# Kernel tuning notes

Hardware: AMD Instinct MI355X
Metric: run time of the kernel (lower is better)

The kernel has to match this reference:

```python
import math
import jax, jax.numpy as jnp
import numpy as np

B, T, C, H = 4, 2048, 1024, 16

def _rope_cos_sin(dim, max_pos):
    half = dim // 2
    pos = jnp.arange(max_pos, dtype=jnp.float32)[:, None]
    freqs = jnp.exp(jnp.arange(half, dtype=jnp.float32) * (-math.log(10000.0) / (half - 1)))[None, :]
    args = pos * freqs  # [T, half]
    return jnp.cos(args), jnp.sin(args)

def _apply_rope(x, cos, sin):
    # x: [B, H, T, D]; pairs (even, odd) along D form complex numbers
    xr = x[..., 0::2]
    xi = x[..., 1::2]
    c = cos[None, None, :, :]
    s = sin[None, None, :, :]
    out_r = xr * c - xi * s
    out_i = xr * s + xi * c
    return jnp.stack([out_r, out_i], axis=-1).reshape(x.shape)

def setup_inputs() -> dict:
    key = jax.random.key(0)
    ks = jax.random.split(key, 9)
    sc = 1.0 / math.sqrt(C)
    return {
        "x": jax.random.normal(ks[0], (B, T, C), jnp.float32),
        "Wq": jax.random.normal(ks[1], (C, C), jnp.float32) * sc,
        "bq": jax.random.normal(ks[2], (C,), jnp.float32) * 0.01,
        "Wk": jax.random.normal(ks[3], (C, C), jnp.float32) * sc,
        "bk": jax.random.normal(ks[4], (C,), jnp.float32) * 0.01,
        "Wv": jax.random.normal(ks[5], (C, C), jnp.float32) * sc,
        "bv": jax.random.normal(ks[6], (C,), jnp.float32) * 0.01,
        "Wp": jax.random.normal(ks[7], (C, C), jnp.float32) * sc,
        "bp": jax.random.normal(ks[8], (C,), jnp.float32) * 0.01,
        "n_head": H,
    }

def reference(x, Wq, bq, Wk, bk, Wv, bv, Wp, bp, n_head):
    Bx, Tx, Cx = x.shape
    D = Cx // n_head
    def heads(w, b):
        return (x @ w + b).reshape(Bx, Tx, n_head, D).transpose(0, 2, 1, 3)  # [B,H,T,D]
    q = heads(Wq, bq)
    k = heads(Wk, bk)
    v = heads(Wv, bv)
    cos, sin = _rope_cos_sin(D, Tx)
    q = _apply_rope(q, cos, sin)
    k = _apply_rope(k, cos, sin)
    att = jnp.einsum("bhtd,bhsd->bhts", q, k) * (1.0 / math.sqrt(D))
    causal = jnp.tril(jnp.ones((Tx, Tx), dtype=bool))
    att = jnp.where(causal[None, None, :, :], att, jnp.float32(-1e10))
    att = jax.nn.softmax(att, axis=-1)
    y = jnp.einsum("bhts,bhsd->bhtd", att, v)
    y = y.transpose(0, 2, 1, 3).reshape(Bx, Tx, Cx)
    return y @ Wp + bp
```

## Files before the change

kernel.cpp:

```cpp
#include <hip/hip_runtime.h>
#include <hip/hip_bf16.h>
#include <stdint.h>

namespace {

constexpr int Bx = 4, Tx = 2048, Cx = 1024, Hx = 16, Dx = 64;
constexpr int Mx = Bx * Tx;

typedef __attribute__((ext_vector_type(8))) short bf16x8;
typedef __attribute__((ext_vector_type(4))) float f32x4;
typedef __attribute__((ext_vector_type(16))) float f32x16;
typedef __attribute__((ext_vector_type(2))) unsigned int u32x2;

__device__ __forceinline__ float b2f(unsigned short u) {
  unsigned int v = ((unsigned int)u) << 16;
  return __builtin_bit_cast(float, v);
}
__device__ __forceinline__ unsigned short f2b(float f) {
  unsigned int v = __builtin_bit_cast(unsigned int, f);
  v += 0x7fffu + ((v >> 16) & 1u);
  return (unsigned short)(v >> 16);
}
__device__ __forceinline__ uint32_t pkbf(float a, float b) {
  __hip_bfloat162 h = __float22bfloat162_rn(float2{a, b});
  uint32_t r;
  __builtin_memcpy(&r, &h, 4);
  return r;
}
__device__ __forceinline__ void pl32swap(uint32_t& a, uint32_t& b) {
  u32x2 r = __builtin_amdgcn_permlane32_swap(a, b, false, false);
  a = r[0];
  b = r[1];
}

#define GLD16(g, lp) __builtin_amdgcn_global_load_lds(                     \
    (__attribute__((address_space(1))) void*)(g),                          \
    (__attribute__((address_space(3))) void*)(lp), 16, 0, 0)

__global__ void ca_cvt(const float* __restrict__ src, unsigned short* __restrict__ dst, int n4) {
  int i = blockIdx.x * blockDim.x + threadIdx.x;
  int stride = gridDim.x * blockDim.x;
  for (; i < n4; i += stride) {
    float4 f = ((const float4*)src)[i];
    ushort4 o;
    o.x = f2b(f.x); o.y = f2b(f.y); o.z = f2b(f.z); o.w = f2b(f.w);
    ((ushort4*)dst)[i] = o;
  }
}

__global__ void ca_wt(const float* __restrict__ W, unsigned short* __restrict__ Wt) {
  __shared__ float tile[32][33];
  int n0 = blockIdx.x * 32, k0 = blockIdx.y * 32;
  int j = threadIdx.x & 31, i = threadIdx.x >> 5;
#pragma unroll
  for (int r = 0; r < 4; ++r)
    tile[i + 8 * r][j] = W[(size_t)(k0 + i + 8 * r) * Cx + n0 + j];
  __syncthreads();
#pragma unroll
  for (int r = 0; r < 4; ++r)
    Wt[(size_t)(n0 + i + 8 * r) * Cx + k0 + j] = f2b(tile[j][i + 8 * r]);
}

__global__ void ca_rtab(float* __restrict__ ct, float* __restrict__ st) {
  int idx = blockIdx.x * blockDim.x + threadIdx.x;
  int t = idx >> 5, i = idx & 31;
  float fr = expf((float)i * -0.29710775393471563f);
  float a = (float)t * fr;
  ct[idx] = cosf(a);
  st[idx] = sinf(a);
}

template <int MODE>
__global__ __launch_bounds__(256) void ca_gemm(
    const unsigned short* __restrict__ A, const unsigned short* __restrict__ Bt,
    const float* __restrict__ b0, const float* __restrict__ b1, const float* __restrict__ b2,
    const float* __restrict__ ctab, const float* __restrict__ stab,
    void* __restrict__ out, int M, int N, int K) {
  __shared__ __align__(16) unsigned short Al[2][128 * 32];
  __shared__ __align__(16) unsigned short Bl[2][128 * 32];
  int tid = threadIdx.x;
  int w = tid >> 6, l = tid & 63;
  int m0 = blockIdx.x * 128, n0 = blockIdx.y * 128;
  int wm = (w >> 1) * 64, wn = (w & 1) * 64;
  f32x4 acc[4][4] = {};

  int lr = l & 15, lk8 = (l >> 4) * 8;
  int srow = w * 32 + (l >> 2), scol = (l & 3) * 8;
  const unsigned short* ga0 = A + (size_t)(m0 + srow) * K + scol;
  const unsigned short* gb0 = Bt + (size_t)(n0 + srow) * K + scol;
  int nk = K / 32;
  auto stage = [&](int kt, int buf) {
    const unsigned short* ga = ga0 + kt * 32;
    const unsigned short* gb = gb0 + kt * 32;
    unsigned short* la = &Al[buf][w * 1024];
    unsigned short* lb = &Bl[buf][w * 1024];
    GLD16(ga, la);
    GLD16(ga + (size_t)16 * K, la + 512);
    GLD16(gb, lb);
    GLD16(gb + (size_t)16 * K, lb + 512);
  };
  stage(0, 0);
  __syncthreads();
  int cur = 0;
  for (int kt = 0; kt < nk; ++kt) {
    if (kt + 1 < nk) stage(kt + 1, cur ^ 1);
    bf16x8 af[4], bfr[4];
#pragma unroll
    for (int mi = 0; mi < 4; ++mi)
      af[mi] = *(const bf16x8*)&Al[cur][(wm + mi * 16 + lr) * 32 + lk8];
#pragma unroll
    for (int ni = 0; ni < 4; ++ni)
      bfr[ni] = *(const bf16x8*)&Bl[cur][(wn + ni * 16 + lr) * 32 + lk8];
#pragma unroll
    for (int mi = 0; mi < 4; ++mi)
#pragma unroll
      for (int ni = 0; ni < 4; ++ni)
        acc[mi][ni] = __builtin_amdgcn_mfma_f32_16x16x32_bf16(af[mi], bfr[ni], acc[mi][ni], 0, 0, 0);
    __syncthreads();
    cur ^= 1;
  }

  int lq4 = (l >> 4) * 4;
  if (MODE == 0) {
    constexpr float SC = 0.18033688011112042f;
    int which = n0 >> 10;
    int nb = n0 & 1023;
    const float* bias = which == 0 ? b0 : (which == 1 ? b1 : b2);
    unsigned short* o = (unsigned short*)out + (size_t)which * M * 1024;
    bool doRope = which < 2;
    float scl = which == 0 ? SC : 1.0f;
#pragma unroll
    for (int mi = 0; mi < 4; ++mi)
#pragma unroll
      for (int ni = 0; ni < 4; ++ni) {
        int ncol = nb + wn + ni * 16 + lr;
        float bv = bias[ncol];
        int j = (ncol & 63) >> 1;
        bool even = (ncol & 1) == 0;
#pragma unroll
        for (int rg = 0; rg < 4; ++rg) {
          int m = m0 + wm + mi * 16 + lq4 + rg;
          float val = acc[mi][ni][rg] + bv;
          if (doRope) {
            int t = m & (Tx - 1);
            float c = ctab[t * 32 + j], s = stab[t * 32 + j];
            float other = __shfl_xor(val, 1);
            float res = even ? (val * c - other * s) : (other * s + val * c);
            val = res * scl;
          }
          o[(size_t)m * 1024 + ncol] = f2b(val);
        }
      }
  } else {
    float* o = (float*)out;
#pragma unroll
    for (int mi = 0; mi < 4; ++mi)
#pragma unroll
      for (int ni = 0; ni < 4; ++ni) {
        int ncol = n0 + wn + ni * 16 + lr;
        float bv = b0[ncol];
#pragma unroll
        for (int rg = 0; rg < 4; ++rg) {
          int m = m0 + wm + mi * 16 + lq4 + rg;
          o[(size_t)m * N + ncol] = acc[mi][ni][rg] + bv;
        }
      }
  }
}

__global__ void ca_vfl(const unsigned short* __restrict__ v, unsigned short* __restrict__ vfl) {
  __shared__ __align__(16) unsigned short tl[64][80];
  int t0 = blockIdx.x * 64;
  int bh = blockIdx.y;
  int b = bh >> 4, h = bh & 15;
  int tid = threadIdx.x;
  const unsigned short* vb = v + (size_t)b * Tx * Cx + h * Dx;
#pragma unroll
  for (int it = 0; it < 2; ++it) {
    int tt = it * 32 + (tid >> 3), d0 = (tid & 7) * 8;
    uint4 x = *(const uint4*)&vb[(size_t)(t0 + tt) * Cx + d0];
    unsigned short* u = (unsigned short*)&x;
#pragma unroll
    for (int jj = 0; jj < 8; ++jj) tl[d0 + jj][tt] = u[jj];
  }
  __syncthreads();
  int l = tid & 63, lo = l & 31, hi = l >> 5;
  int g = tid >> 6, tloc = g >> 1, kc = g & 1;
  int tglob = (t0 >> 5) + tloc;
  unsigned short* vo = vfl + ((size_t)bh * 64 + tglob) * 2048;
#pragma unroll
  for (int dc = 0; dc < 2; ++dc) {
    int j = dc * 2 + kc;
    uint4 x = *(const uint4*)&tl[dc * 32 + lo][tloc * 32 + hi * 8 + kc * 16];
    *(uint4*)(vo + j * 512 + l * 8) = x;
  }
}

__global__ __launch_bounds__(64) void ca_kfl(
    const unsigned short* __restrict__ k, unsigned short* __restrict__ kfl) {
  int l = threadIdx.x & 63;
  int bh = blockIdx.x, t = blockIdx.y;
  int b = bh >> 4, h = bh & 15;
  int lo = l & 31, hi = l >> 5;
  const unsigned short* kr = k + (size_t)b * Tx * Cx + h * Dx + (size_t)(t * 32 + lo) * Cx + hi * 8;
  unsigned short* ko = kfl + ((size_t)bh * 64 + t) * 2048;
#pragma unroll
  for (int c = 0; c < 4; ++c) {
    uint4 x = *(const uint4*)(kr + c * 16);
    *(uint4*)(ko + c * 512 + l * 8) = x;
  }
}

__global__ __launch_bounds__(64) void ca_attn(
    const unsigned short* __restrict__ q, const unsigned short* __restrict__ kfl,
    const unsigned short* __restrict__ vfl, unsigned short* __restrict__ y) {
  __shared__ uint32_t els[32][33];
  int l = threadIdx.x & 63;
  int bh = blockIdx.x;
  int qt = (int)gridDim.y - 1 - (int)blockIdx.y;
  int b = bh >> 4, h16 = bh & 15;
  const unsigned short* qp = q + (size_t)b * Tx * Cx + h16 * Dx;
  const unsigned short* kb = kfl + (size_t)bh * 64 * 2048 + l * 8;
  const unsigned short* vb = vfl + (size_t)bh * 64 * 2048 + l * 8;
  int lo = l & 31, hi = l >> 5;
  constexpr float SHIFT = 20.0f;
  const uint32_t one2 = 0x3F803F80u;
  uint4 onesw{one2, one2, one2, one2};
  bf16x8 ONES = __builtin_bit_cast(bf16x8, onesw);

  int qbase = qt * 32;

  bf16x8 qf[4];
  {
    const unsigned short* qr = qp + (size_t)(qbase + lo) * Cx + hi * 8;
#pragma unroll
    for (int c = 0; c < 4; ++c) qf[c] = *(const bf16x8*)(qr + c * 16);
  }

  f32x16 acc0 = {}, acc1 = {}, sacc = {};
  int nt = qt + 1;

  uint4 rk[4], rv[4];
  auto loadK = [&](int t) {
#pragma unroll
    for (int c = 0; c < 4; ++c) rk[c] = *(const uint4*)(kb + t * 2048 + c * 512);
  };
  auto loadV = [&](int t) {
#pragma unroll
    for (int j = 0; j < 4; ++j) rv[j] = *(const uint4*)(vb + t * 2048 + j * 512);
  };
  loadK(0);
  loadV(0);

  for (int t = 0; t < nt; ++t) {
    bf16x8 kf[4], vf[4];
#pragma unroll
    for (int c = 0; c < 4; ++c) kf[c] = __builtin_bit_cast(bf16x8, rk[c]);
#pragma unroll
    for (int c = 0; c < 4; ++c) vf[c] = __builtin_bit_cast(bf16x8, rv[c]);
    if (t + 1 < nt) { loadK(t + 1); loadV(t + 1); }

    __builtin_amdgcn_s_setprio(1);
    f32x16 s = {};
    s = __builtin_amdgcn_mfma_f32_32x32x16_bf16(kf[0], qf[0], s, 0, 0, 0);
    s = __builtin_amdgcn_mfma_f32_32x32x16_bf16(kf[1], qf[1], s, 0, 0, 0);
    s = __builtin_amdgcn_mfma_f32_32x32x16_bf16(kf[2], qf[2], s, 0, 0, 0);
    s = __builtin_amdgcn_mfma_f32_32x32x16_bf16(kf[3], qf[3], s, 0, 0, 0);
    __builtin_amdgcn_s_setprio(0);

    float p[16];
    if (t == nt - 1) {
#pragma unroll
      for (int r = 0; r < 16; ++r) {
        int kvr = (r & 3) + 8 * (r >> 2) + 4 * hi;
        p[r] = (kvr > lo) ? 0.f : exp2f(s[r] - SHIFT);
      }
    } else {
#pragma unroll
      for (int r = 0; r < 16; ++r) p[r] = exp2f(s[r] - SHIFT);
    }

    uint32_t pk[8];
#pragma unroll
    for (int i = 0; i < 8; ++i) pk[i] = pkbf(p[2 * i], p[2 * i + 1]);
    pl32swap(pk[0], pk[2]);
    pl32swap(pk[1], pk[3]);
    pl32swap(pk[4], pk[6]);
    pl32swap(pk[5], pk[7]);
    uint4 xw{pk[0], pk[1], pk[2], pk[3]}, yw{pk[4], pk[5], pk[6], pk[7]};
    bf16x8 PB0 = __builtin_bit_cast(bf16x8, xw);
    bf16x8 PB1 = __builtin_bit_cast(bf16x8, yw);
    __builtin_amdgcn_s_setprio(1);
    acc0 = __builtin_amdgcn_mfma_f32_32x32x16_bf16(vf[0], PB0, acc0, 0, 0, 0);
    acc1 = __builtin_amdgcn_mfma_f32_32x32x16_bf16(vf[2], PB0, acc1, 0, 0, 0);
    sacc = __builtin_amdgcn_mfma_f32_32x32x16_bf16(ONES, PB0, sacc, 0, 0, 0);
    acc0 = __builtin_amdgcn_mfma_f32_32x32x16_bf16(vf[1], PB1, acc0, 0, 0, 0);
    acc1 = __builtin_amdgcn_mfma_f32_32x32x16_bf16(vf[3], PB1, acc1, 0, 0, 0);
    sacc = __builtin_amdgcn_mfma_f32_32x32x16_bf16(ONES, PB1, sacc, 0, 0, 0);
    __builtin_amdgcn_s_setprio(0);
  }

  float rl = __builtin_amdgcn_rcpf(sacc[0]);
#pragma unroll
  for (int dc = 0; dc < 2; ++dc) {
    f32x16 a = dc ? acc1 : acc0;
#pragma unroll
    for (int i = 0; i < 8; ++i) {
      uint32_t pkd = pkbf(a[2 * i] * rl, a[2 * i + 1] * rl);
      int d2 = (i & 1) + 4 * (i >> 1) + 2 * hi + dc * 16;
      els[lo][d2] = pkd;
    }
  }
  __syncthreads();
  unsigned short* yp = y + (size_t)b * Tx * Cx + h16 * Dx;
#pragma unroll
  for (int pp = 0; pp < 16; ++pp) {
    int qr = 2 * pp + hi;
    uint32_t val = els[qr][lo];
    *(uint32_t*)(yp + (size_t)(qbase + qr) * Cx + lo * 2) = val;
  }
}

}

extern "C" void kernel_launch(void* const* d_in, const int* in_sizes, int n_in,
                              void* d_out, int out_size, void* d_ws, size_t ws_size,
                              hipStream_t stream) {
  const float* x = (const float*)d_in[0];
  const float* Wq = (const float*)d_in[1];
  const float* bq = (const float*)d_in[2];
  const float* Wk = (const float*)d_in[3];
  const float* bk = (const float*)d_in[4];
  const float* Wv = (const float*)d_in[5];
  const float* bv = (const float*)d_in[6];
  const float* Wp = (const float*)d_in[7];
  const float* bp = (const float*)d_in[8];

  unsigned short* xb = (unsigned short*)d_ws;
  unsigned short* wt = xb + (size_t)Mx * Cx;
  float* ct = (float*)(wt + (size_t)4 * Cx * Cx);
  float* st = ct + Tx * 32;
  unsigned short* qb = (unsigned short*)(st + Tx * 32);
  unsigned short* kb = qb + (size_t)Mx * Cx;
  unsigned short* vb = kb + (size_t)Mx * Cx;
  unsigned short* vT = vb + (size_t)Mx * Cx;
  unsigned short* yb = vT + (size_t)Mx * Cx;
  unsigned short* kfl = yb + (size_t)Mx * Cx;
  unsigned short* vfl = kfl + (size_t)64 * 64 * 2048;

  ca_cvt<<<dim3(2048), dim3(256), 0, stream>>>(x, xb, Mx * Cx / 4);
  ca_wt<<<dim3(32, 32), dim3(256), 0, stream>>>(Wq, wt + (size_t)0 * Cx * Cx);
  ca_wt<<<dim3(32, 32), dim3(256), 0, stream>>>(Wk, wt + (size_t)1 * Cx * Cx);
  ca_wt<<<dim3(32, 32), dim3(256), 0, stream>>>(Wv, wt + (size_t)2 * Cx * Cx);
  ca_wt<<<dim3(32, 32), dim3(256), 0, stream>>>(Wp, wt + (size_t)3 * Cx * Cx);
  ca_rtab<<<dim3(Tx * 32 / 256), dim3(256), 0, stream>>>(ct, st);

  ca_gemm<0><<<dim3(64, 24), dim3(256), 0, stream>>>(xb, wt, bq, bk, bv, ct, st, qb, Mx, 3072, Cx);
  ca_vfl<<<dim3(Tx / 64, Bx * Hx), dim3(256), 0, stream>>>(vb, vfl);
  ca_kfl<<<dim3(64, 64), dim3(64), 0, stream>>>(kb, kfl);
  ca_attn<<<dim3(64, 64), dim3(64), 0, stream>>>(qb, kfl, vfl, yb);
  ca_gemm<1><<<dim3(64, 8), dim3(256), 0, stream>>>(yb, wt + (size_t)3 * Cx * Cx, bp,
                                                    nullptr, nullptr, nullptr, nullptr,
                                                    d_out, Mx, Cx, Cx);
}
```

Baseline: 217.5 us.

## Replace QKV projection GEMM with 256x256-tile 8-wave kernel using direct-to-LDS loads

```diff
diff --git a/kernel.cpp b/kernel.cpp
--- a/kernel.cpp
+++ b/kernel.cpp
@@ -70,12 +70,130 @@
   st[idx] = sinf(a);
 }
 
-template <int MODE>
-__global__ __launch_bounds__(256) void ca_gemm(
+__global__ __launch_bounds__(512, 1) void ca_gemm8(
     const unsigned short* __restrict__ A, const unsigned short* __restrict__ Bt,
     const float* __restrict__ b0, const float* __restrict__ b1, const float* __restrict__ b2,
     const float* __restrict__ ctab, const float* __restrict__ stab,
-    void* __restrict__ out, int M, int N, int K) {
+    unsigned short* __restrict__ out) {
+  extern __shared__ unsigned short lds8[];
+  unsigned short* ldsA = lds8;
+  unsigned short* ldsB = lds8 + 32768;
+
+  int tid = threadIdx.x;
+  int w = tid >> 6, l = tid & 63;
+  int wr = w >> 2, wc = w & 3;
+
+  int bid = (int)blockIdx.x;
+  int wgid = (bid & 7) * 48 + (bid >> 3);
+  int m0 = (wgid & 31) * 256;
+  int n0 = (wgid >> 5) * 256;
+
+  const unsigned short* aSrc = A + (size_t)(m0 + w * 8 + (l >> 3)) * Cx + (((l & 7) ^ (l >> 3)) * 8);
+  const unsigned short* bSrc = Bt + (size_t)(n0 + w * 8 + (l >> 3)) * Cx + (((l & 7) ^ (l >> 3)) * 8);
+  int dstRow = w * 8;
+
+  auto stageQ = [&](int ktn, int q, int buf) {
+    int half = q & 1;
+    size_t roff = (size_t)(half * 128) * Cx + ktn * 64;
+    if (q < 2) {
+      unsigned short* d = ldsA + buf * 16384 + (half * 128 + dstRow) * 64;
+      GLD16(aSrc + roff, d);
+      GLD16(aSrc + roff + (size_t)64 * Cx, d + 64 * 64);
+    } else {
+      unsigned short* d = ldsB + buf * 16384 + (half * 128 + dstRow) * 64;
+      GLD16(bSrc + roff, d);
+      GLD16(bSrc + roff + (size_t)64 * Cx, d + 64 * 64);
+    }
+  };
+
+  f32x4 acc[8][4] = {};
+  int rA = wr * 128 + (l & 15);
+  int rB = wc * 64 + (l & 15);
+  int gp0 = ((l >> 4)) ^ (l & 7);
+  int gp1 = (4 + (l >> 4)) ^ (l & 7);
+
+#pragma unroll
+  for (int q = 0; q < 4; ++q) stageQ(0, q, 0);
+
+  constexpr int NK = 16;
+  for (int kt = 0; kt < NK; ++kt) {
+    int cb = kt & 1, nb2 = cb ^ 1;
+    const unsigned short* bufA = ldsA + cb * 16384;
+    const unsigned short* bufB = ldsB + cb * 16384;
+    bf16x8 bfr[4][2];
+#pragma unroll
+    for (int q = 0; q < 4; ++q) {
+      if (kt + 1 < NK) stageQ(kt + 1, q, nb2);
+      if (q == 0) {
+        if (kt + 1 < NK) {
+          asm volatile("s_waitcnt vmcnt(2)" ::: "memory");
+        } else {
+          asm volatile("s_waitcnt vmcnt(0)" ::: "memory");
+        }
+        __builtin_amdgcn_sched_barrier(0);
+        __builtin_amdgcn_s_barrier();
+#pragma unroll
+        for (int ni = 0; ni < 4; ++ni) {
+          bfr[ni][0] = *(const bf16x8*)&bufB[(rB + ni * 16) * 64 + gp0 * 8];
+          bfr[ni][1] = *(const bf16x8*)&bufB[(rB + ni * 16) * 64 + gp1 * 8];
+        }
+      }
+      bf16x8 af[2][2];
+#pragma unroll
+      for (int mi2 = 0; mi2 < 2; ++mi2) {
+        af[mi2][0] = *(const bf16x8*)&bufA[(rA + (q * 2 + mi2) * 16) * 64 + gp0 * 8];
+        af[mi2][1] = *(const bf16x8*)&bufA[(rA + (q * 2 + mi2) * 16) * 64 + gp1 * 8];
+      }
+      __builtin_amdgcn_s_setprio(1);
+#pragma unroll
+      for (int mi2 = 0; mi2 < 2; ++mi2)
+#pragma unroll
+        for (int ni = 0; ni < 4; ++ni) {
+          acc[q * 2 + mi2][ni] =
+              __builtin_amdgcn_mfma_f32_16x16x32_bf16(af[mi2][0], bfr[ni][0], acc[q * 2 + mi2][ni], 0, 0, 0);
+          acc[q * 2 + mi2][ni] =
+              __builtin_amdgcn_mfma_f32_16x16x32_bf16(af[mi2][1], bfr[ni][1], acc[q * 2 + mi2][ni], 0, 0, 0);
+        }
+      __builtin_amdgcn_s_setprio(0);
+      __builtin_amdgcn_s_barrier();
+    }
+  }
+
+  constexpr float SC = 0.18033688011112042f;
+  int lr15 = l & 15, lq4 = (l >> 4) * 4;
+  int which = n0 >> 10;
+  int nbo = n0 & 1023;
+  const float* bias = which == 0 ? b0 : (which == 1 ? b1 : b2);
+  unsigned short* o = out + (size_t)which * Mx * 1024;
+  bool doRope = which < 2;
+  float scl = which == 0 ? SC : 1.0f;
+#pragma unroll
+  for (int mi = 0; mi < 8; ++mi)
+#pragma unroll
+    for (int ni = 0; ni < 4; ++ni) {
+      int ncol = nbo + wc * 64 + ni * 16 + lr15;
+      float bv = bias[ncol];
+      int j = (ncol & 63) >> 1;
+      bool even = (ncol & 1) == 0;
+#pragma unroll
+      for (int rg = 0; rg < 4; ++rg) {
+        int m = m0 + wr * 128 + mi * 16 + lq4 + rg;
+        float val = acc[mi][ni][rg] + bv;
+        if (doRope) {
+          int t = m & (Tx - 1);
+          float c = ctab[t * 32 + j], s = stab[t * 32 + j];
+          float other = __shfl_xor(val, 1);
+          float res = even ? (val * c - other * s) : (other * s + val * c);
+          val = res * scl;
+        }
+        o[(size_t)m * 1024 + ncol] = f2b(val);
+      }
+    }
+}
+
+__global__ __launch_bounds__(256) void ca_gemmp(
+    const unsigned short* __restrict__ A, const unsigned short* __restrict__ Bt,
+    const float* __restrict__ b0, float* __restrict__ out, int M, int N, int K) {
   __shared__ __align__(16) unsigned short Al[2][128 * 32];
   __shared__ __align__(16) unsigned short Bl[2][128 * 32];
   int tid = threadIdx.x;
@@ -119,53 +237,20 @@
     __syncthreads();
     cur ^= 1;
   }
-
   int lq4 = (l >> 4) * 4;
-  if (MODE == 0) {
-    constexpr float SC = 0.18033688011112042f;
-    int which = n0 >> 10;
-    int nb = n0 & 1023;
-    const float* bias = which == 0 ? b0 : (which == 1 ? b1 : b2);
-    unsigned short* o = (unsigned short*)out + (size_t)which * M * 1024;
-    bool doRope = which < 2;
-    float scl = which == 0 ? SC : 1.0f;
-#pragma unroll
-    for (int mi = 0; mi < 4; ++mi)
-#pragma unroll
-      for (int ni = 0; ni < 4; ++ni) {
-        int ncol = nb + wn + ni * 16 + lr;
-        float bv = bias[ncol];
-        int j = (ncol & 63) >> 1;
-        bool even = (ncol & 1) == 0;
-#pragma unroll
-        for (int rg = 0; rg < 4; ++rg) {
-          int m = m0 + wm + mi * 16 + lq4 + rg;
-          float val = acc[mi][ni][rg] + bv;
-          if (doRope) {
-            int t = m & (Tx - 1);
-            float c = ctab[t * 32 + j], s = stab[t * 32 + j];
-            float other = __shfl_xor(val, 1);
-            float res = even ? (val * c - other * s) : (other * s + val * c);
-            val = res * scl;
-          }
-          o[(size_t)m * 1024 + ncol] = f2b(val);
-        }
+  float* o = out;
+#pragma unroll
+  for (int mi = 0; mi < 4; ++mi)
+#pragma unroll
+    for (int ni = 0; ni < 4; ++ni) {
+      int ncol = n0 + wn + ni * 16 + lr;
+      float bv = b0[ncol];
+#pragma unroll
+      for (int rg = 0; rg < 4; ++rg) {
+        int m = m0 + wm + mi * 16 + lq4 + rg;
+        o[(size_t)m * N + ncol] = acc[mi][ni][rg] + bv;
       }
-  } else {
-    float* o = (float*)out;
-#pragma unroll
-    for (int mi = 0; mi < 4; ++mi)
-#pragma unroll
-      for (int ni = 0; ni < 4; ++ni) {
-        int ncol = n0 + wn + ni * 16 + lr;
-        float bv = b0[ncol];
-#pragma unroll
-        for (int rg = 0; rg < 4; ++rg) {
-          int m = m0 + wm + mi * 16 + lq4 + rg;
-          o[(size_t)m * N + ncol] = acc[mi][ni][rg] + bv;
-        }
-      }
-  }
+    }
 }
 
 __global__ void ca_vfl(const unsigned short* __restrict__ v, unsigned short* __restrict__ vfl) {
@@ -355,11 +440,10 @@
   ca_wt<<<dim3(32, 32), dim3(256), 0, stream>>>(Wp, wt + (size_t)3 * Cx * Cx);
   ca_rtab<<<dim3(Tx * 32 / 256), dim3(256), 0, stream>>>(ct, st);
 
-  ca_gemm<0><<<dim3(64, 24), dim3(256), 0, stream>>>(xb, wt, bq, bk, bv, ct, st, qb, Mx, 3072, Cx);
+  ca_gemm8<<<dim3(384), dim3(512), 131072, stream>>>(xb, wt, bq, bk, bv, ct, st, qb);
   ca_vfl<<<dim3(Tx / 64, Bx * Hx), dim3(256), 0, stream>>>(vb, vfl);
   ca_kfl<<<dim3(64, 64), dim3(64), 0, stream>>>(kb, kfl);
   ca_attn<<<dim3(64, 64), dim3(64), 0, stream>>>(qb, kfl, vfl, yb);
-  ca_gemm<1><<<dim3(64, 8), dim3(256), 0, stream>>>(yb, wt + (size_t)3 * Cx * Cx, bp,
-                                                    nullptr, nullptr, nullptr, nullptr,
-                                                    d_out, Mx, Cx, Cx);
-}
+  ca_gemmp<<<dim3(64, 8), dim3(256), 0, stream>>>(yb, wt + (size_t)3 * Cx * Cx, bp,
+                                                  (float*)d_out, Mx, Cx, Cx);
+}
```

Result: slower. 246.8 us (+13.5%).
